# Performance work log

Measured on AMD Instinct MI355X. Metric: run time of the kernel, lower is better.

The kernel has to match this reference:

```python
import jax, jax.numpy as jnp
import numpy as np

D = 1024
H = 16
L = 2048
B = 2
EPS = 1e-5


def setup_inputs() -> dict:
    key = jax.random.key(0)
    ks = jax.random.split(key, 12)
    s = 0.02
    return {
        "x": jax.random.normal(ks[0], (B, L, D), dtype=jnp.float32),
        "ln1_w": jnp.ones((D,), jnp.float32),
        "ln1_b": jnp.zeros((D,), jnp.float32),
        "ln2_w": jnp.ones((D,), jnp.float32),
        "ln2_b": jnp.zeros((D,), jnp.float32),
        "attn_w": jax.random.normal(ks[1], (D, 3 * D), jnp.float32) * s,
        "attn_b": jnp.zeros((3 * D,), jnp.float32),
        "proj_w": jax.random.normal(ks[2], (D, D), jnp.float32) * s,
        "proj_b": jnp.zeros((D,), jnp.float32),
        "fc1_w": jax.random.normal(ks[3], (D, 4 * D), jnp.float32) * s,
        "fc1_b": jnp.zeros((4 * D,), jnp.float32),
        "fc2_w": jax.random.normal(ks[4], (4 * D, D), jnp.float32) * s,
        "fc2_b": jnp.zeros((D,), jnp.float32),
    }


def layernorm(x, w, b):
    mu = jnp.mean(x, axis=-1, keepdims=True)
    var = jnp.mean(jnp.square(x - mu), axis=-1, keepdims=True)
    return (x - mu) * jax.lax.rsqrt(var + EPS) * w + b


def reference(x, ln1_w, ln1_b, ln2_w, ln2_b, attn_w, attn_b,
              proj_w, proj_b, fc1_w, fc1_b, fc2_w, fc2_b):
    Bsz, Lq, C = x.shape
    hd = C // H

    # --- attention branch ---
    h = layernorm(x, ln1_w, ln1_b)
    qkv = h @ attn_w + attn_b                      # [B, L, 3C]
    q, k, v = jnp.split(qkv, 3, axis=-1)
    q = q.reshape(Bsz, Lq, H, hd).transpose(0, 2, 1, 3)  # [B, H, L, hd]
    k = k.reshape(Bsz, Lq, H, hd).transpose(0, 2, 1, 3)
    v = v.reshape(Bsz, Lq, H, hd).transpose(0, 2, 1, 3)

    # NOTE: original scales by 1/sqrt(embedding_dim), not sqrt(head_dim)
    att = jnp.einsum('bhqd,bhkd->bhqk', q, k) / jnp.sqrt(jnp.float32(C))
    causal = jnp.tril(jnp.ones((Lq, Lq), dtype=bool))
    att = jnp.where(causal[None, None], att, jnp.float32(-jnp.inf))
    att = jax.nn.softmax(att, axis=-1)
    y = jnp.einsum('bhqk,bhkd->bhqd', att, v)      # [B, H, L, hd]
    y = y.transpose(0, 2, 1, 3).reshape(Bsz, Lq, C)
    y = y @ proj_w + proj_b
    x = x + y

    # --- MLP branch ---
    h = layernorm(x, ln2_w, ln2_b)
    h = jax.nn.gelu(h @ fc1_w + fc1_b, approximate=False)
    h = h @ fc2_w + fc2_b
    return x + h
```

## Files before the change

### kernel.cpp

```cpp
#include <hip/hip_runtime.h>

#define Bsz 2
#define Lq  2048
#define Dm  1024
#define Hh  16

typedef __attribute__((ext_vector_type(8))) short bf16x8;
typedef __attribute__((ext_vector_type(4))) float f32x4;

#define MFMA16(a, b, c) __builtin_amdgcn_mfma_f32_16x16x32_bf16((a), (b), (c), 0, 0, 0)
#define EXP2F(x) __builtin_amdgcn_exp2f(x)

__device__ __forceinline__ short f2bf(float f) {
    union { float f; unsigned u; } v; v.f = f;
    unsigned r = v.u + 0x7fffu + ((v.u >> 16) & 1u);
    return (short)(r >> 16);
}

__device__ __forceinline__ float bf2f(unsigned short s) {
    union { float f; unsigned u; } t; t.u = ((unsigned)s) << 16;
    return t.f;
}

__device__ __forceinline__ int pk2(float a, float b) {
    union { float f; unsigned u; } ua, ub; ua.f = a; ub.f = b;
    return (int)((ua.u >> 16) | (ub.u & 0xffff0000u));
}

__device__ __forceinline__ void gload16(const void* g, void* l) {
    __builtin_amdgcn_global_load_lds((const __attribute__((address_space(1))) void*)g,
                                     (__attribute__((address_space(3))) void*)l,
                                     16, 0, 0);
}

__global__ __launch_bounds__(256) void prologue_all(
    const float* __restrict__ attnw, const float* __restrict__ projw,
    const float* __restrict__ fc1w,  const float* __restrict__ fc2w,
    short* __restrict__ attnwT, short* __restrict__ projwT,
    short* __restrict__ fc1wT,  short* __restrict__ fc2wT,
    const float* __restrict__ x, const float* __restrict__ lnw,
    const float* __restrict__ lnb, short* __restrict__ lnout) {
    int id = blockIdx.x;
    if (id >= 12288) {
        const int row = id - 12288;
        const int tid = threadIdx.x;
        const float4 v = ((const float4*)(x + (size_t)row * 1024))[tid];
        float s = v.x + v.y + v.z + v.w;
        float q = v.x * v.x + v.y * v.y + v.z * v.z + v.w * v.w;
        for (int off = 32; off > 0; off >>= 1) {
            s += __shfl_down(s, off);
            q += __shfl_down(q, off);
        }
        __shared__ float red[8];
        const int wave = tid >> 6;
        if ((tid & 63) == 0) { red[wave] = s; red[wave + 4] = q; }
        __syncthreads();
        s = red[0] + red[1] + red[2] + red[3];
        q = red[4] + red[5] + red[6] + red[7];
        const float mu = s * (1.0f / 1024.0f);
        const float var = q * (1.0f / 1024.0f) - mu * mu;
        const float rstd = rsqrtf(var + 1e-5f);
        const float4 wv = ((const float4*)lnw)[tid];
        const float4 bv = ((const float4*)lnb)[tid];
        short4 o;
        o.x = f2bf((v.x - mu) * rstd * wv.x + bv.x);
        o.y = f2bf((v.y - mu) * rstd * wv.y + bv.y);
        o.z = f2bf((v.z - mu) * rstd * wv.z + bv.z);
        o.w = f2bf((v.w - mu) * rstd * wv.w + bv.w);
        ((short4*)(lnout + (size_t)row * 1024))[tid] = o;
        return;
    }
    const float* W; short* Wt; int K, N, bx, by;
    if (id < 3072)      { W = attnw; Wt = attnwT; K = 1024; N = 3072; bx = id % 96;  by = id / 96; }
    else if (id < 4096) { id -= 3072; W = projw; Wt = projwT; K = 1024; N = 1024; bx = id & 31; by = id >> 5; }
    else if (id < 8192) { id -= 4096; W = fc1w;  Wt = fc1wT;  K = 1024; N = 4096; bx = id & 127; by = id >> 7; }
    else                { id -= 8192; W = fc2w;  Wt = fc2wT;  K = 4096; N = 1024; bx = id & 31; by = id >> 5; }
    __shared__ float t[32][33];
    const int n0 = bx * 32, k0 = by * 32;
    const int tx = threadIdx.x & 31, ty = threadIdx.x >> 5;
#pragma unroll
    for (int i = 0; i < 4; i++)
        t[ty + i * 8][tx] = W[(size_t)(k0 + ty + i * 8) * N + n0 + tx];
    __syncthreads();
#pragma unroll
    for (int i = 0; i < 4; i++)
        Wt[(size_t)(n0 + ty + i * 8) * K + k0 + tx] = f2bf(t[tx][ty + i * 8]);
}

template <int EP>
__global__ __launch_bounds__(256, 4) void gemm_bt(
    const short* __restrict__ A, const short* __restrict__ Bt,
    const float* __restrict__ bias, int N, int K,
    short* __restrict__ qd, short* __restrict__ kd, short* __restrict__ vtd,
    short* __restrict__ outb) {
    __shared__ short As[128 * 64];
    __shared__ short Bs[128 * 64];
    const int tid = threadIdx.x;
    const int lane = tid & 63, w = tid >> 6;
    const int l16 = lane & 15, quad = lane >> 4;
    const int wr = (w & 1) * 64, wc = (w >> 1) * 64;
    const int n = blockIdx.x;
    const int row0 = ((n & 7) * 4 + ((n >> 3) & 3)) * 128;
    const int col0 = (n >> 5) * 128;
    const int srow = lane >> 3;
    const int scol = ((lane & 7) ^ srow) * 8;

    f32x4 acc[4][4];
    const f32x4 z = {0.f, 0.f, 0.f, 0.f};
#pragma unroll
    for (int i = 0; i < 4; i++)
#pragma unroll
        for (int j = 0; j < 4; j++) acc[i][j] = z;

    const short* pA[4];
    const short* pB[4];
#pragma unroll
    for (int g = 0; g < 4; g++) {
        pA[g] = A + (size_t)(row0 + w * 32 + g * 8 + srow) * K + scol;
        pB[g] = Bt + (size_t)(col0 + w * 32 + g * 8 + srow) * K + scol;
    }

    for (int k0 = 0; k0 < K; k0 += 64) {
#pragma unroll
        for (int g = 0; g < 4; g++) {
            gload16(pA[g], &As[(w * 32 + g * 8) * 64]);
            gload16(pB[g], &Bs[(w * 32 + g * 8) * 64]);
            pA[g] += 64; pB[g] += 64;
        }
        __syncthreads();
#pragma unroll
        for (int kk = 0; kk < 2; kk++) {
            const int rsl = ((kk * 4 + quad) ^ (l16 & 7)) * 8;
            bf16x8 a[4], bb[4];
#pragma unroll
            for (int i = 0; i < 4; i++) a[i] = *(const bf16x8*)&As[(wr + i * 16 + l16) * 64 + rsl];
#pragma unroll
            for (int j = 0; j < 4; j++) bb[j] = *(const bf16x8*)&Bs[(wc + j * 16 + l16) * 64 + rsl];
#pragma unroll
            for (int i = 0; i < 4; i++)
#pragma unroll
                for (int j = 0; j < 4; j++) acc[i][j] = MFMA16(a[i], bb[j], acc[i][j]);
        }
        __syncthreads();
    }

    float bz[4];
#pragma unroll
    for (int j = 0; j < 4; j++) bz[j] = bias[col0 + wc + j * 16 + l16];

#pragma unroll
    for (int i = 0; i < 4; i++) {
#pragma unroll
        for (int r = 0; r < 4; r++) {
            const int grow = row0 + wr + i * 16 + quad * 4 + r;
#pragma unroll
            for (int j = 0; j < 4; j++) {
                const int gcol = col0 + wc + j * 16 + l16;
                const float v = acc[i][j][r] + bz[j];
                if constexpr (EP == 0) {
                    const int b = grow >> 11, l = grow & 2047;
                    const int sec = gcol >> 10, wi = gcol & 1023;
                    const int h = wi >> 6, d = wi & 63;
                    if (sec == 2) {
                        vtd[(((size_t)b * Hh + h) * 64 + d) * Lq + l] = f2bf(v);
                    } else {
                        short* dst = sec ? kd : qd;
                        dst[(((size_t)b * Hh + h) * Lq + l) * 64 + d] = f2bf(v);
                    }
                } else {
                    const float g = 0.5f * v * (1.0f + erff(v * 0.70710678118f));
                    outb[(size_t)grow * N + gcol] = f2bf(g);
                }
            }
        }
    }
}

__global__ __launch_bounds__(256, 4) void gemm_sk(
    const short* __restrict__ A, const short* __restrict__ Bt, int K, int zbits,
    short* __restrict__ Cp) {
    __shared__ short As[128 * 64];
    __shared__ short Bs[128 * 64];
    const int tid = threadIdx.x;
    const int lane = tid & 63, w = tid >> 6;
    const int l16 = lane & 15, quad = lane >> 4;
    const int wr = (w & 1) * 64, wc = (w >> 1) * 64;
    const int n = blockIdx.x;
    const int xcd = n & 7, t = n >> 3;
    const int col = t & 7, u = t >> 3;
    const int c = xcd * (4 << zbits) + u;
    const int zsl = c & ((1 << zbits) - 1);
    const int row0 = (c >> zbits) * 128, col0 = col * 128;
    const int KS = K >> zbits;
    const int kbeg = zsl * KS, kend = kbeg + KS;
    const int srow = lane >> 3;
    const int scol = ((lane & 7) ^ srow) * 8;

    f32x4 acc[4][4];
    const f32x4 z = {0.f, 0.f, 0.f, 0.f};
#pragma unroll
    for (int i = 0; i < 4; i++)
#pragma unroll
        for (int j = 0; j < 4; j++) acc[i][j] = z;

    const short* pA[4];
    const short* pB[4];
#pragma unroll
    for (int g = 0; g < 4; g++) {
        pA[g] = A + (size_t)(row0 + w * 32 + g * 8 + srow) * K + kbeg + scol;
        pB[g] = Bt + (size_t)(col0 + w * 32 + g * 8 + srow) * K + kbeg + scol;
    }

    for (int k0 = kbeg; k0 < kend; k0 += 64) {
#pragma unroll
        for (int g = 0; g < 4; g++) {
            gload16(pA[g], &As[(w * 32 + g * 8) * 64]);
            gload16(pB[g], &Bs[(w * 32 + g * 8) * 64]);
            pA[g] += 64; pB[g] += 64;
        }
        __syncthreads();
#pragma unroll
        for (int kk = 0; kk < 2; kk++) {
            const int rsl = ((kk * 4 + quad) ^ (l16 & 7)) * 8;
            bf16x8 a[4], bb[4];
#pragma unroll
            for (int i = 0; i < 4; i++) a[i] = *(const bf16x8*)&As[(wr + i * 16 + l16) * 64 + rsl];
#pragma unroll
            for (int j = 0; j < 4; j++) bb[j] = *(const bf16x8*)&Bs[(wc + j * 16 + l16) * 64 + rsl];
#pragma unroll
            for (int i = 0; i < 4; i++)
#pragma unroll
                for (int j = 0; j < 4; j++) acc[i][j] = MFMA16(a[i], bb[j], acc[i][j]);
        }
        __syncthreads();
    }

    short* cp = Cp + (size_t)zsl * 4096 * 1024;
#pragma unroll
    for (int i = 0; i < 4; i++) {
#pragma unroll
        for (int r = 0; r < 4; r++) {
            const int grow = row0 + wr + i * 16 + quad * 4 + r;
#pragma unroll
            for (int j = 0; j < 4; j++) {
                const int gcol = col0 + wc + j * 16 + l16;
                cp[(size_t)grow * 1024 + gcol] = f2bf(acc[i][j][r]);
            }
        }
    }
}

__global__ __launch_bounds__(256) void sk_reduce(const short* __restrict__ Cp, int S,
                                                 const float* __restrict__ res,
                                                 const float* __restrict__ bias,
                                                 float* __restrict__ out) {
    const int row = blockIdx.x, tid = threadIdx.x;
    const size_t base = (size_t)row * 1024 + tid * 4;
    float4 a = ((const float4*)(res + (size_t)row * 1024))[tid];
    const float4 bz = ((const float4*)bias)[tid];
    a.x += bz.x; a.y += bz.y; a.z += bz.z; a.w += bz.w;
    for (int s = 0; s < S; s++) {
        const ushort4 c = *(const ushort4*)(Cp + (size_t)s * 4096 * 1024 + base);
        a.x += bf2f(c.x); a.y += bf2f(c.y); a.z += bf2f(c.z); a.w += bf2f(c.w);
    }
    *(float4*)(out + base) = a;
}

__global__ __launch_bounds__(256) void sk_reduce_ln(const short* __restrict__ Cp, int S,
                                                    const float* __restrict__ res,
                                                    const float* __restrict__ bias,
                                                    const float* __restrict__ lnw,
                                                    const float* __restrict__ lnb,
                                                    float* __restrict__ xout,
                                                    short* __restrict__ hout) {
    const int row = blockIdx.x, tid = threadIdx.x;
    const size_t base = (size_t)row * 1024 + tid * 4;
    float4 a = ((const float4*)(res + (size_t)row * 1024))[tid];
    const float4 bz = ((const float4*)bias)[tid];
    a.x += bz.x; a.y += bz.y; a.z += bz.z; a.w += bz.w;
    for (int s = 0; s < S; s++) {
        const ushort4 c = *(const ushort4*)(Cp + (size_t)s * 4096 * 1024 + base);
        a.x += bf2f(c.x); a.y += bf2f(c.y); a.z += bf2f(c.z); a.w += bf2f(c.w);
    }
    *(float4*)(xout + base) = a;
    float sm = a.x + a.y + a.z + a.w;
    float qs = a.x * a.x + a.y * a.y + a.z * a.z + a.w * a.w;
    for (int off = 32; off > 0; off >>= 1) {
        sm += __shfl_down(sm, off);
        qs += __shfl_down(qs, off);
    }
    __shared__ float red[8];
    const int wave = tid >> 6;
    if ((tid & 63) == 0) { red[wave] = sm; red[wave + 4] = qs; }
    __syncthreads();
    sm = red[0] + red[1] + red[2] + red[3];
    qs = red[4] + red[5] + red[6] + red[7];
    const float mu = sm * (1.0f / 1024.0f);
    const float var = qs * (1.0f / 1024.0f) - mu * mu;
    const float rstd = rsqrtf(var + 1e-5f);
    const float4 wv = ((const float4*)lnw)[tid];
    const float4 bv = ((const float4*)lnb)[tid];
    short4 o;
    o.x = f2bf((a.x - mu) * rstd * wv.x + bv.x);
    o.y = f2bf((a.y - mu) * rstd * wv.y + bv.y);
    o.z = f2bf((a.z - mu) * rstd * wv.z + bv.z);
    o.w = f2bf((a.w - mu) * rstd * wv.w + bv.w);
    ((short4*)(hout + (size_t)row * 1024))[tid] = o;
}

#define KP 72
__global__ __launch_bounds__(256, 2) void attn_kernel(const short* __restrict__ Q,
                                                      const short* __restrict__ Kb,
                                                      const short* __restrict__ Vt,
                                                      short* __restrict__ Y) {
    const int tid = threadIdx.x;
    const int lane = tid & 63, wave = tid >> 6;
    const int l16 = lane & 15, quad = lane >> 4;
    const int n = blockIdx.x;
    const int xcd = n & 7, m = n >> 3;
    const int bh = xcd * 4 + (m & 3);
    const int mm = (m & 31) >> 2;
    const int qblk = (m < 32) ? (15 - mm) : mm;
    const int qw = qblk * 128 + wave * 32;

    const short* qg = Q + ((size_t)bh * Lq + qw) * 64;
    const short* kg = Kb + (size_t)bh * Lq * 64;
    const short* vg = Vt + (size_t)bh * 64 * Lq;

    __shared__ short sK[2][64 * 64];
    __shared__ short sV[2][64 * 64];
    __shared__ short sP[4][32 * KP];
    short* wpP = sP[wave];

    const float c1 = 0.0450842213f;

    bf16x8 qf[2][2];
#pragma unroll
    for (int c = 0; c < 2; c++)
#pragma unroll
        for (int d = 0; d < 2; d++) {
            bf16x8 v = *(const bf16x8*)(qg + (c * 16 + l16) * 64 + d * 32 + quad * 8);
            bf16x8 r;
#pragma unroll
            for (int i = 0; i < 8; i++) {
                union { float f; unsigned u; } t;
                t.u = ((unsigned)(unsigned short)v[i]) << 16;
                r[i] = f2bf(t.f * c1);
            }
            qf[c][d] = r;
        }

    f32x4 o[4][2];
    const f32x4 z = {0.f, 0.f, 0.f, 0.f};
#pragma unroll
    for (int j = 0; j < 4; j++)
#pragma unroll
        for (int c = 0; c < 2; c++) o[j][c] = z;
    float l_i[2] = {0.f, 0.f};

    const int srow8 = lane >> 3;
    const int sslot = ((lane & 7) ^ srow8) * 8;
    const int r0 = wave * 16;
    const int nst = 2 * qblk + 2;

    auto stage = [&](int s) {
        const int p = s & 1;
        const int kb = s * 64;
        gload16(kg + (size_t)(kb + r0 + srow8) * 64 + sslot,     &sK[p][r0 * 64]);
        gload16(kg + (size_t)(kb + r0 + 8 + srow8) * 64 + sslot, &sK[p][(r0 + 8) * 64]);
        gload16(vg + (size_t)(r0 + srow8) * Lq + kb + sslot,     &sV[p][r0 * 64]);
        gload16(vg + (size_t)(r0 + 8 + srow8) * Lq + kb + sslot, &sV[p][(r0 + 8) * 64]);
    };

    stage(0);

    for (int s = 0; s < nst; ++s) {
        const int p = s & 1;
        __syncthreads();
        bf16x8 kf[4][2];
#pragma unroll
        for (int kt = 0; kt < 4; kt++)
#pragma unroll
            for (int d = 0; d < 2; d++)
                kf[kt][d] = *(const bf16x8*)&sK[p][(kt * 16 + l16) * 64 +
                                                   (((d * 4 + quad) ^ (l16 & 7)) * 8)];
        if (s + 1 < nst) stage(s + 1);

        f32x4 st[4][2];
#pragma unroll
        for (int kt = 0; kt < 4; kt++)
#pragma unroll
            for (int c = 0; c < 2; c++) {
                st[kt][c] = MFMA16(kf[kt][0], qf[c][0], z);
                st[kt][c] = MFMA16(kf[kt][1], qf[c][1], st[kt][c]);
            }

        const int rel = s * 64 - qblk * 128 - wave * 32;
        if (rel > -64) {
#pragma unroll
            for (int kt = 0; kt < 4; kt++)
#pragma unroll
                for (int c = 0; c < 2; c++)
#pragma unroll
                    for (int r = 0; r < 4; r++) {
                        const int krel = rel + kt * 16 + quad * 4 + r - c * 16;
                        if (krel > l16) st[kt][c][r] = -1e30f;
                    }
        }

#pragma unroll
        for (int c = 0; c < 2; c++) {
            float pv[4][4], rs = 0.f;
#pragma unroll
            for (int kt = 0; kt < 4; kt++)
#pragma unroll
                for (int r = 0; r < 4; r++) {
                    pv[kt][r] = EXP2F(st[kt][c][r]);
                    rs += pv[kt][r];
                }
            l_i[c] += rs;
            short* wp = wpP + (c * 16 + l16) * KP;
#pragma unroll
            for (int kt = 0; kt < 4; kt++) {
                int2 pw; pw.x = pk2(pv[kt][0], pv[kt][1]); pw.y = pk2(pv[kt][2], pv[kt][3]);
                *(int2*)(wp + kt * 16 + quad * 4) = pw;
            }
        }

        bf16x8 pf[2][2];
#pragma unroll
        for (int c = 0; c < 2; c++) {
            pf[c][0] = *(const bf16x8*)(wpP + (c * 16 + l16) * KP + quad * 8);
            pf[c][1] = *(const bf16x8*)(wpP + (c * 16 + l16) * KP + 32 + quad * 8);
        }
#pragma unroll
        for (int j = 0; j < 4; j++) {
            const bf16x8 v0 = *(const bf16x8*)&sV[p][(j * 16 + l16) * 64 +
                                                     ((quad ^ (l16 & 7)) * 8)];
            const bf16x8 v1 = *(const bf16x8*)&sV[p][(j * 16 + l16) * 64 +
                                                     (((4 + quad) ^ (l16 & 7)) * 8)];
#pragma unroll
            for (int c = 0; c < 2; c++) {
                o[j][c] = MFMA16(v0, pf[c][0], o[j][c]);
                o[j][c] = MFMA16(v1, pf[c][1], o[j][c]);
            }
        }
    }

    const int b = bh >> 4, h = bh & 15;
#pragma unroll
    for (int c = 0; c < 2; c++) {
        float ls = l_i[c];
        ls += __shfl_xor(ls, 16);
        ls += __shfl_xor(ls, 32);
        const float inv = 1.0f / ls;
        const size_t base = ((size_t)b * Lq + qw + c * 16 + l16) * 1024 + h * 64;
#pragma unroll
        for (int j = 0; j < 4; j++) {
            short4 s4;
            s4.x = f2bf(o[j][c][0] * inv);
            s4.y = f2bf(o[j][c][1] * inv);
            s4.z = f2bf(o[j][c][2] * inv);
            s4.w = f2bf(o[j][c][3] * inv);
            *(short4*)(Y + base + j * 16 + quad * 4) = s4;
        }
    }
}

extern "C" void kernel_launch(void* const* d_in, const int* in_sizes, int n_in,
                              void* d_out, int out_size, void* d_ws, size_t ws_size,
                              hipStream_t stream) {
    (void)in_sizes; (void)n_in; (void)out_size; (void)ws_size;
    const float* x     = (const float*)d_in[0];
    const float* ln1w  = (const float*)d_in[1];
    const float* ln1b  = (const float*)d_in[2];
    const float* ln2w  = (const float*)d_in[3];
    const float* ln2b  = (const float*)d_in[4];
    const float* attnw = (const float*)d_in[5];
    const float* attnb = (const float*)d_in[6];
    const float* projw = (const float*)d_in[7];
    const float* projb = (const float*)d_in[8];
    const float* fc1w  = (const float*)d_in[9];
    const float* fc1b  = (const float*)d_in[10];
    const float* fc2w  = (const float*)d_in[11];
    const float* fc2b  = (const float*)d_in[12];
    float* out = (float*)d_out;

    char* ws = (char*)d_ws;
    size_t off = 0;
    auto alloc = [&](size_t bytes) {
        void* p = ws + off;
        off += (bytes + 255) & ~(size_t)255;
        return p;
    };
    short* attnwT = (short*)alloc(3072ull * 1024 * 2);
    short* projwT = (short*)alloc(1024ull * 1024 * 2);
    short* fc1wT  = (short*)alloc(4096ull * 1024 * 2);
    short* fc2wT  = (short*)alloc(1024ull * 4096 * 2);
    short* hbuf   = (short*)alloc(4096ull * 1024 * 2);
    short* qbuf   = (short*)alloc(4096ull * 1024 * 2);
    short* kbuf   = (short*)alloc(4096ull * 1024 * 2);
    short* vtbuf  = (short*)alloc(4096ull * 1024 * 2);
    short* ybuf   = (short*)alloc(4096ull * 1024 * 2);
    float* x1     = (float*)alloc(4096ull * 1024 * 4);
    short* Cp     = (short*)alloc(4ull * 4096 * 1024 * 2);
    short* hh = qbuf;

    prologue_all<<<16384, 256, 0, stream>>>(attnw, projw, fc1w, fc2w,
                                            attnwT, projwT, fc1wT, fc2wT,
                                            x, ln1w, ln1b, hbuf);

    gemm_bt<0><<<768, 256, 0, stream>>>(hbuf, attnwT, attnb, 3072, 1024,
                                        qbuf, kbuf, vtbuf, nullptr);
    attn_kernel<<<512, 256, 0, stream>>>(qbuf, kbuf, vtbuf, ybuf);
    gemm_sk<<<512, 256, 0, stream>>>(ybuf, projwT, 1024, 1, Cp);
    sk_reduce_ln<<<4096, 256, 0, stream>>>(Cp, 2, x, projb, ln2w, ln2b, x1, hbuf);

    gemm_bt<2><<<1024, 256, 0, stream>>>(hbuf, fc1wT, fc1b, 4096, 1024,
                                         nullptr, nullptr, nullptr, hh);
    gemm_sk<<<1024, 256, 0, stream>>>(hh, fc2wT, 4096, 2, Cp);
    sk_reduce<<<4096, 256, 0, stream>>>(Cp, 4, x1, fc2b, out);
}
```

Baseline: 317.8 us.

## Replace split-K partial buffers and reduce kernels with fp32 atomic accumulation

Split-K GEMM slices now atomically add their fp32 partial sums straight into the residual output, instead of writing bf16 partials that a separate kernel reduces. The residual plus bias is pre-initialised earlier: x+proj_b in the prologue, and x1+fc2_b in the LN2 kernel. This removes one reduce kernel and the partial-buffer traffic. In exchange it adds many scattered atomic adds, and summation order becomes nondeterministic.

```diff
diff --git a/kernel.cpp b/kernel.cpp
--- a/kernel.cpp
+++ b/kernel.cpp
@@ -39,12 +39,17 @@
     short* __restrict__ attnwT, short* __restrict__ projwT,
     short* __restrict__ fc1wT,  short* __restrict__ fc2wT,
     const float* __restrict__ x, const float* __restrict__ lnw,
-    const float* __restrict__ lnb, short* __restrict__ lnout) {
+    const float* __restrict__ lnb, short* __restrict__ lnout,
+    const float* __restrict__ projb, float* __restrict__ x1) {
     int id = blockIdx.x;
     if (id >= 12288) {
         const int row = id - 12288;
         const int tid = threadIdx.x;
         const float4 v = ((const float4*)(x + (size_t)row * 1024))[tid];
+        const float4 pb = ((const float4*)projb)[tid];
+        float4 xi;
+        xi.x = v.x + pb.x; xi.y = v.y + pb.y; xi.z = v.z + pb.z; xi.w = v.w + pb.w;
+        ((float4*)(x1 + (size_t)row * 1024))[tid] = xi;
         float s = v.x + v.y + v.z + v.w;
         float q = v.x * v.x + v.y * v.y + v.z * v.z + v.w * v.w;
         for (int off = 32; off > 0; off >>= 1) {
@@ -178,7 +183,7 @@
 
 __global__ __launch_bounds__(256, 4) void gemm_sk(
     const short* __restrict__ A, const short* __restrict__ Bt, int K, int zbits,
-    short* __restrict__ Cp) {
+    float* __restrict__ Dst) {
     __shared__ short As[128 * 64];
     __shared__ short Bs[128 * 64];
     const int tid = threadIdx.x;
@@ -235,7 +240,6 @@
         __syncthreads();
     }
 
-    short* cp = Cp + (size_t)zsl * 4096 * 1024;
 #pragma unroll
     for (int i = 0; i < 4; i++) {
 #pragma unroll
@@ -244,45 +248,24 @@
 #pragma unroll
             for (int j = 0; j < 4; j++) {
                 const int gcol = col0 + wc + j * 16 + l16;
-                cp[(size_t)grow * 1024 + gcol] = f2bf(acc[i][j][r]);
+                unsafeAtomicAdd(&Dst[(size_t)grow * 1024 + gcol], acc[i][j][r]);
             }
         }
     }
 }
 
-__global__ __launch_bounds__(256) void sk_reduce(const short* __restrict__ Cp, int S,
-                                                 const float* __restrict__ res,
-                                                 const float* __restrict__ bias,
-                                                 float* __restrict__ out) {
+__global__ __launch_bounds__(256) void ln2_fc2init(const float* __restrict__ x1,
+                                                   const float* __restrict__ lnw,
+                                                   const float* __restrict__ lnb,
+                                                   const float* __restrict__ fc2b,
+                                                   short* __restrict__ hout,
+                                                   float* __restrict__ out) {
     const int row = blockIdx.x, tid = threadIdx.x;
-    const size_t base = (size_t)row * 1024 + tid * 4;
-    float4 a = ((const float4*)(res + (size_t)row * 1024))[tid];
-    const float4 bz = ((const float4*)bias)[tid];
-    a.x += bz.x; a.y += bz.y; a.z += bz.z; a.w += bz.w;
-    for (int s = 0; s < S; s++) {
-        const ushort4 c = *(const ushort4*)(Cp + (size_t)s * 4096 * 1024 + base);
-        a.x += bf2f(c.x); a.y += bf2f(c.y); a.z += bf2f(c.z); a.w += bf2f(c.w);
-    }
-    *(float4*)(out + base) = a;
-}
-
-__global__ __launch_bounds__(256) void sk_reduce_ln(const short* __restrict__ Cp, int S,
-                                                    const float* __restrict__ res,
-                                                    const float* __restrict__ bias,
-                                                    const float* __restrict__ lnw,
-                                                    const float* __restrict__ lnb,
-                                                    float* __restrict__ xout,
-                                                    short* __restrict__ hout) {
-    const int row = blockIdx.x, tid = threadIdx.x;
-    const size_t base = (size_t)row * 1024 + tid * 4;
-    float4 a = ((const float4*)(res + (size_t)row * 1024))[tid];
-    const float4 bz = ((const float4*)bias)[tid];
-    a.x += bz.x; a.y += bz.y; a.z += bz.z; a.w += bz.w;
-    for (int s = 0; s < S; s++) {
-        const ushort4 c = *(const ushort4*)(Cp + (size_t)s * 4096 * 1024 + base);
-        a.x += bf2f(c.x); a.y += bf2f(c.y); a.z += bf2f(c.z); a.w += bf2f(c.w);
-    }
-    *(float4*)(xout + base) = a;
+    const float4 a = ((const float4*)(x1 + (size_t)row * 1024))[tid];
+    const float4 fb = ((const float4*)fc2b)[tid];
+    float4 oi;
+    oi.x = a.x + fb.x; oi.y = a.y + fb.y; oi.z = a.z + fb.z; oi.w = a.w + fb.w;
+    ((float4*)(out + (size_t)row * 1024))[tid] = oi;
     float sm = a.x + a.y + a.z + a.w;
     float qs = a.x * a.x + a.y * a.y + a.z * a.z + a.w * a.w;
     for (int off = 32; off > 0; off >>= 1) {
@@ -503,21 +486,19 @@
     short* vtbuf  = (short*)alloc(4096ull * 1024 * 2);
     short* ybuf   = (short*)alloc(4096ull * 1024 * 2);
     float* x1     = (float*)alloc(4096ull * 1024 * 4);
-    short* Cp     = (short*)alloc(4ull * 4096 * 1024 * 2);
     short* hh = qbuf;
 
     prologue_all<<<16384, 256, 0, stream>>>(attnw, projw, fc1w, fc2w,
                                             attnwT, projwT, fc1wT, fc2wT,
-                                            x, ln1w, ln1b, hbuf);
+                                            x, ln1w, ln1b, hbuf, projb, x1);
 
     gemm_bt<0><<<768, 256, 0, stream>>>(hbuf, attnwT, attnb, 3072, 1024,
                                         qbuf, kbuf, vtbuf, nullptr);
     attn_kernel<<<512, 256, 0, stream>>>(qbuf, kbuf, vtbuf, ybuf);
-    gemm_sk<<<512, 256, 0, stream>>>(ybuf, projwT, 1024, 1, Cp);
-    sk_reduce_ln<<<4096, 256, 0, stream>>>(Cp, 2, x, projb, ln2w, ln2b, x1, hbuf);
+    gemm_sk<<<512, 256, 0, stream>>>(ybuf, projwT, 1024, 1, x1);
+    ln2_fc2init<<<4096, 256, 0, stream>>>(x1, ln2w, ln2b, fc2b, hbuf, out);
 
     gemm_bt<2><<<1024, 256, 0, stream>>>(hbuf, fc1wT, fc1b, 4096, 1024,
                                          nullptr, nullptr, nullptr, hh);
-    gemm_sk<<<1024, 256, 0, stream>>>(hh, fc2wT, 4096, 2, Cp);
-    sk_reduce<<<4096, 256, 0, stream>>>(Cp, 4, x1, fc2b, out);
-}
+    gemm_sk<<<1024, 256, 0, stream>>>(hh, fc2wT, 4096, 2, out);
+}
```

After: 353.3 us. 11.2% more time.
